# Performance work log

Hardware: AMD Instinct MI355X
Metric: run time of the kernel (lower is better)

## Reference

```python
import jax, jax.numpy as jnp
import numpy as np

E = 128   # embedding_dim
H = 4     # num_heads
D = E * H # internal width = 512 (MHA head_dim = E)
B = 512
N = 128


def setup_inputs() -> dict:
    key = jax.random.key(0)
    ks = jax.random.split(key, 16)
    s = lambda fan_in: 1.0 / np.sqrt(fan_in)
    u = lambda k, shape, sc: jax.random.uniform(k, shape, jnp.float32, -sc, sc)
    inp = {
        "x": jax.random.normal(ks[0], (B, N, E), jnp.float32),
        "weights": jax.random.uniform(ks[1], (B, N, 1), jnp.float32),
        # self.embedding: Linear(E, D)
        "emb_W": u(ks[2], (D, E), s(E)), "emb_b": u(ks[3], (D,), s(E)),
        # outer W_q/W_k/W_v: Linear(D, D)
        "wq_W": u(ks[4], (D, D), s(D)), "wq_b": u(ks[5], (D,), s(D)),
        "wk_W": u(ks[6], (D, D), s(D)), "wk_b": u(ks[7], (D,), s(D)),
        "wv_W": u(ks[8], (D, D), s(D)), "wv_b": u(ks[9], (D,), s(D)),
        # nn.MultiheadAttention packed in-projection (out_proj is irrelevant:
        # its output is discarded, only att_weights are used)
        "in_proj_W": u(ks[10], (3 * D, D), s(D)),
        "in_proj_b": jnp.zeros((3 * D,), jnp.float32),
        # LayerNorm(D)
        "ln_g": jnp.ones((D,), jnp.float32), "ln_b": jnp.zeros((D,), jnp.float32),
        # self.out: Linear(D, E)
        "out_W": u(ks[11], (E, D), s(D)), "out_b": u(ks[12], (E,), s(D)),
    }
    return inp


def reference(x, weights, emb_W, emb_b, wq_W, wq_b, wk_W, wk_b, wv_W, wv_b,
              in_proj_W, in_proj_b, ln_g, ln_b, out_W, out_b):
    # x: [B, N, E] -> embedded [B, N, D]
    xe = x @ emb_W.T + emb_b
    # key_padding_mask: rows of xe that are all-zero
    pad = jnp.sum(jnp.abs(xe), axis=-1) == 0.0              # [B, N] bool

    # outer projections
    q_in = xe @ wq_W.T + wq_b
    k_in = xe @ wk_W.T + wk_b
    v_in = xe @ wv_W.T + wv_b                               # [B, N, D]

    # MHA internal packed in-projection
    Wq, Wk, Wv = in_proj_W[:D], in_proj_W[D:2 * D], in_proj_W[2 * D:]
    bq, bk, bv = in_proj_b[:D], in_proj_b[D:2 * D], in_proj_b[2 * D:]
    hd = D // H  # head_dim = E
    to_heads = lambda t: t.reshape(t.shape[0], t.shape[1], H, hd).transpose(0, 2, 1, 3)
    q = to_heads(q_in @ Wq.T + bq)                          # [B, H, N, hd]
    k = to_heads(k_in @ Wk.T + bk)

    scores = jnp.einsum('bhie,bhje->bhij', q, k) / jnp.sqrt(jnp.float32(hd))
    scores = jnp.where(pad[:, None, None, :], -jnp.inf, scores)
    attn = jax.nn.softmax(scores, axis=-1)                  # [B, H, N, N]
    att_weights = jnp.mean(attn, axis=1)                    # averaged over heads [B, N, N]

    # external reweighting + renormalization
    att_weights = att_weights * jnp.swapaxes(weights, -2, -1)  # [B,N,N]*[B,1,N]
    att_weights = att_weights / jnp.sum(att_weights, axis=-1, keepdims=True)

    # re-apply to outer V projection (MHA's own output is discarded)
    att_output = jnp.einsum('bij,bjd->bid', att_weights, v_in)

    h = xe + jax.nn.softplus(att_output)
    mu = jnp.mean(h, axis=-1, keepdims=True)
    var = jnp.mean((h - mu) ** 2, axis=-1, keepdims=True)
    h = (h - mu) / jnp.sqrt(var + 1e-5) * ln_g + ln_b
    return h @ out_W.T + out_b                              # [B, N, E]
```

## Files before the change

kernel.cpp:

```cpp
#include <hip/hip_runtime.h>
#include <stdint.h>


typedef __attribute__((ext_vector_type(8))) __bf16 bf16x8;
typedef __attribute__((ext_vector_type(8))) uint16_t u16x8;
typedef __attribute__((ext_vector_type(4))) float f32x4;

__device__ __forceinline__ float b2f(uint16_t h) {
  union { uint32_t u; float f; } c; c.u = ((uint32_t)h) << 16; return c.f;
}
__device__ __forceinline__ uint16_t f2b(float f) {
  __bf16 h = (__bf16)f;
  union { __bf16 b; uint16_t u; } c; c.b = h; return c.u;
}
__device__ __forceinline__ void gld16(void* lds, const void* g) {
  __builtin_amdgcn_global_load_lds(
      (const __attribute__((address_space(1))) uint32_t*)(g),
      (__attribute__((address_space(3))) uint32_t*)(lds),
      16, 0, 0);
}

#define MFMA16(a, b, c) __builtin_amdgcn_mfma_f32_16x16x32_bf16((a), (b), (c), 0, 0, 0)

__global__ __launch_bounds__(256) void pack_all(
    const float* __restrict__ x,
    const float* __restrict__ emb_W, const float* __restrict__ wq_W,
    const float* __restrict__ wk_W, const float* __restrict__ wv_W,
    const float* __restrict__ ipW, const float* __restrict__ out_W,
    const float* __restrict__ ln_g,
    uint16_t* __restrict__ x_bf,
    uint16_t* __restrict__ embW2, uint16_t* __restrict__ wqW_bf,
    uint16_t* __restrict__ wkW_bf, uint16_t* __restrict__ Wvc,
    uint16_t* __restrict__ ip_bf, uint16_t* __restrict__ owW_bf) {
  int i = blockIdx.x * 256 + threadIdx.x;
  if (i < 2097152) {
    float4 v = ((const float4*)x)[i];
    ushort4 o;
    o.x = f2b(v.x); o.y = f2b(v.y); o.z = f2b(v.z); o.w = f2b(v.w);
    ((ushort4*)x_bf)[i] = o;
    return;
  }
  int i2 = i - 2097152;
  if (i2 >= 360448) return;
  if (i2 >= 344064) {
    const int off = i2 - 344064;
    float4 v = ((const float4*)out_W)[off];
    const int base = off * 4;
    ushort4 o;
    o.x = f2b(v.x * ln_g[(base + 0) & 511]);
    o.y = f2b(v.y * ln_g[(base + 1) & 511]);
    o.z = f2b(v.z * ln_g[(base + 2) & 511]);
    o.w = f2b(v.w * ln_g[(base + 3) & 511]);
    ((ushort4*)owW_bf)[off] = o;
    return;
  }
  const float* src; uint16_t* dst; int off;
  if (i2 < 16384)       { src = emb_W; dst = embW2;  off = i2; }
  else if (i2 < 81920)  { src = wq_W;  dst = wqW_bf; off = i2 - 16384; }
  else if (i2 < 147456) { src = wk_W;  dst = wkW_bf; off = i2 - 81920; }
  else if (i2 < 212992) { src = wv_W;  dst = Wvc;    off = i2 - 147456; }
  else                  { src = ipW;   dst = ip_bf;  off = i2 - 212992; }
  float4 v = ((const float4*)src)[off];
  ushort4 o;
  o.x = f2b(v.x); o.y = f2b(v.y); o.z = f2b(v.z); o.w = f2b(v.w);
  ((ushort4*)dst)[off] = o;
}

__global__ __launch_bounds__(256) void bias_stage1(
    const float* __restrict__ wq_W, const float* __restrict__ wk_W,
    const float* __restrict__ wv_W, const float* __restrict__ emb_b,
    const float* __restrict__ wq_b, const float* __restrict__ wk_b,
    const float* __restrict__ wv_b,
    float* __restrict__ t1q, float* __restrict__ t1k, float* __restrict__ bve,
    float* __restrict__ pad_init, float* __restrict__ biasE,
    float* __restrict__ ssum, float* __restrict__ ssq) {
  const int gid = blockIdx.x * 256 + threadIdx.x;
  if (gid < 65536) { pad_init[gid] = 0.f; ssum[gid] = 0.f; ssq[gid] = 0.f; }
  if (gid < 512) biasE[gid] = emb_b[gid];
  const int t = threadIdx.x, l = t & 63, w = t >> 6;
  const int sel = blockIdx.x >> 7;
  const int row = (blockIdx.x & 127) * 4 + w;
  const float* Wbig = sel == 0 ? wq_W : (sel == 1 ? wk_W : wv_W);
  const float* b2   = sel == 0 ? wq_b : (sel == 1 ? wk_b : wv_b);
  float* out        = sel == 0 ? t1q  : (sel == 1 ? t1k  : bve);
  float s = 0.f;
  #pragma unroll
  for (int j = 0; j < 8; ++j) {
    int c = j * 64 + l;
    s += Wbig[(size_t)row * 512 + c] * emb_b[c];
  }
  #pragma unroll
  for (int m = 1; m < 64; m <<= 1) s += __shfl_xor(s, m);
  if (l == 0) out[row] = s + b2[row];
}

__global__ __launch_bounds__(256) void bias_stage2(
    const float* __restrict__ ipW, const float* __restrict__ ipb,
    const float* __restrict__ t1q, const float* __restrict__ t1k,
    float* __restrict__ bqe, float* __restrict__ bke,
    const float* __restrict__ out_W, const float* __restrict__ ln_g,
    const float* __restrict__ ln_b, const float* __restrict__ out_b,
    float* __restrict__ u, float* __restrict__ v) {
  const int t = threadIdx.x, l = t & 63, w = t >> 6;
  const int blk = blockIdx.x;
  if (blk < 256) {
    const int sel = blk >> 7;
    const int row = (blk & 127) * 4 + w;
    const float* Wbig = ipW + (size_t)sel * 262144;
    const float* b1   = sel == 0 ? t1q : t1k;
    const float* b2   = ipb + sel * 512;
    float* out        = sel == 0 ? bqe : bke;
    float s = 0.f;
    #pragma unroll
    for (int j = 0; j < 8; ++j) {
      int c = j * 64 + l;
      s += Wbig[(size_t)row * 512 + c] * b1[c];
    }
    #pragma unroll
    for (int m = 1; m < 64; m <<= 1) s += __shfl_xor(s, m);
    if (l == 0) out[row] = s + b2[row];
  } else {
    const int r4 = (blk - 256) * 4 + w;
    const int row = r4 & 127;
    const float* src = (r4 < 128) ? ln_g : ln_b;
    float s = 0.f;
    #pragma unroll
    for (int j = 0; j < 8; ++j) {
      int c = j * 64 + l;
      s += out_W[(size_t)row * 512 + c] * src[c];
    }
    #pragma unroll
    for (int m = 1; m < 64; m <<= 1) s += __shfl_xor(s, m);
    if (l == 0) {
      if (r4 < 128) u[row] = s;
      else v[row] = s + out_b[row];
    }
  }
}

template <int BIAS_MODE, bool PAD_ACC, bool HV>
__global__ __launch_bounds__(256) void gemm_btp_kernel(
    const uint16_t* __restrict__ A, long long sA,
    const uint16_t* __restrict__ W, long long sW,
    const float* __restrict__ bias, long long sBias,
    uint16_t* __restrict__ C, long long sC,
    int mIter, float* __restrict__ padout,
    const uint16_t* __restrict__ xein, float* __restrict__ ssum,
    float* __restrict__ ssq) {
  __shared__ uint16_t Ws[2][128 * 64];
  __shared__ uint16_t As[2][128 * 64];
  const int t = threadIdx.x, l = t & 63, w = t >> 6;
  const int wr = w >> 1, wc = w & 1, l15 = l & 15, hi = l >> 4;
  const int gx = gridDim.x, gy = gridDim.y;
  const int nwg = gx * gy * gridDim.z;
  const int lin = blockIdx.x + gx * (blockIdx.y + gy * blockIdx.z);
  const int cpx = nwg >> 3;
  const int sw = (nwg & 7) ? lin : ((lin & 7) * cpx + (lin >> 3));
  const int ntile = sw % gx;
  const int rest = sw / gx;
  const int mg = rest % gy, bz = rest / gy;
  const uint16_t* Ab = A + (size_t)bz * sA;
  const uint16_t* Wb = W + (size_t)bz * sW;
  uint16_t* Cb = C + (size_t)bz * sC;
  const float* biasb = bias + (size_t)bz * sBias;
  const int srow = t >> 3;
  const int schunk = (t & 7) * 8;
  const int gchunk = (((t & 7) ^ (srow & 7)) * 8);
  const int rowB0 = ntile * 128;
  #pragma unroll
  for (int kt = 0; kt < 2; ++kt)
    #pragma unroll
    for (int i = 0; i < 4; ++i) {
      const int r = i * 32 + srow;
      gld16(&Ws[kt][r * 64 + schunk], Wb + (size_t)(rowB0 + r) * 128 + kt * 64 + gchunk);
    }
  auto stageA = [&](int u) {
    const int rowA0 = (mg * mIter + (u >> 1)) * 128;
    const int kb = (u & 1) << 6;
    #pragma unroll
    for (int i = 0; i < 4; ++i) {
      const int r = i * 32 + srow;
      gld16(&As[u & 1][r * 64 + schunk], Ab + (size_t)(rowA0 + r) * 128 + kb + gchunk);
    }
  };
  const int rsw = (l15 & 7);
  stageA(0);
  const int U = mIter * 2;
  f32x4 acc[4][4];
  for (int u = 0; u < U; ++u) {
    const int kt = u & 1;
    if (kt == 0) {
      #pragma unroll
      for (int m = 0; m < 4; ++m)
        #pragma unroll
        for (int n = 0; n < 4; ++n) acc[m][n] = (f32x4){0.f, 0.f, 0.f, 0.f};
    }
    if (u + 1 < U) {
      stageA(u + 1);
      asm volatile("s_waitcnt vmcnt(4)" ::: "memory");
    } else {
      asm volatile("s_waitcnt vmcnt(0)" ::: "memory");
    }
    __builtin_amdgcn_s_barrier();
    asm volatile("" ::: "memory");
    #pragma unroll
    for (int ks = 0; ks < 2; ++ks) {
      const int gck = ((ks * 4 + hi) ^ rsw) * 8;
      bf16x8 a[4], bb[4];
      #pragma unroll
      for (int m = 0; m < 4; ++m)
        a[m] = *(const bf16x8*)&As[kt][(wr * 64 + m * 16 + l15) * 64 + gck];
      #pragma unroll
      for (int n = 0; n < 4; ++n)
        bb[n] = *(const bf16x8*)&Ws[kt][(wc * 64 + n * 16 + l15) * 64 + gck];
      #pragma unroll
      for (int m = 0; m < 4; ++m)
        #pragma unroll
        for (int n = 0; n < 4; ++n) acc[m][n] = MFMA16(bb[n], a[m], acc[m][n]);
    }
    asm volatile("" ::: "memory");
    __builtin_amdgcn_s_barrier();
    if (kt == 1) {
      const int rowA0 = (mg * mIter + (u >> 1)) * 128;
      #pragma unroll
      for (int m = 0; m < 4; ++m) {
        const int row = rowA0 + wr * 64 + m * 16 + l15;
        float padp = 0.f, hs = 0.f, hq = 0.f;
        #pragma unroll
        for (int n = 0; n < 4; ++n) {
          const int colb = rowB0 + wc * 64 + n * 16 + hi * 4;
          union { ushort4 v; uint16_t e[4]; } o, xv;
          if constexpr (HV)
            xv.v = *(const ushort4*)&xein[(size_t)row * 512 + colb];
          #pragma unroll
          for (int r = 0; r < 4; ++r) {
            float rv = acc[m][n][r];
            if constexpr (BIAS_MODE == 1) rv += biasb[colb + r];
            if constexpr (PAD_ACC) padp += fabsf(rv);
            if constexpr (HV) {
              const float sp = fmaxf(rv, 0.f) + __logf(1.f + __expf(-fabsf(rv)));
              const float hvv = b2f(xv.e[r]) + sp;
              hs += hvv;
              hq += hvv * hvv;
              o.e[r] = f2b(hvv);
            } else {
              o.e[r] = f2b(rv);
            }
          }
          *(ushort4*)&Cb[(size_t)row * 512 + colb] = o.v;
        }
        if constexpr (PAD_ACC) {
          if (bz == 0) {
            padp += __shfl_xor(padp, 16);
            padp += __shfl_xor(padp, 32);
            if (l < 16) atomicAdd(padout + row, padp);
          }
        }
        if constexpr (HV) {
          hs += __shfl_xor(hs, 16); hs += __shfl_xor(hs, 32);
          hq += __shfl_xor(hq, 16); hq += __shfl_xor(hq, 32);
          if (l < 16) {
            atomicAdd(ssum + row, hs);
            atomicAdd(ssq + row, hq);
          }
        }
      }
    }
  }
}

template <typename OT, int BIAS_MODE, bool LN>
__global__ __launch_bounds__(256) void gemm_bt_kernel(
    const uint16_t* __restrict__ A, long long sA,
    const uint16_t* __restrict__ W, long long sW,
    const float* __restrict__ bias, long long sBias,
    OT* __restrict__ C, long long sC, int N, int K,
    const float* __restrict__ ssum, const float* __restrict__ ssq,
    const float* __restrict__ uarr, const float* __restrict__ varr) {
  __shared__ uint16_t As[2][128 * 64];
  __shared__ uint16_t Bs[2][128 * 64];
  const int t = threadIdx.x, l = t & 63, w = t >> 6;
  const int wr = w >> 1, wc = w & 1, l15 = l & 15, hi = l >> 4;
  const int gx = gridDim.x, gy = gridDim.y;
  const int nwg = gx * gy * gridDim.z;
  const int lin = blockIdx.x + gx * (blockIdx.y + gy * blockIdx.z);
  const int cpx = nwg >> 3;
  const int sw = (nwg & 7) ? lin : ((lin & 7) * cpx + (lin >> 3));
  const int ntile = sw % gx;
  const int rest = sw / gx;
  const int mtile = rest % gy, bz = rest / gy;
  const uint16_t* Ab = A + (size_t)bz * sA;
  const uint16_t* Wb = W + (size_t)bz * sW;
  OT* Cb = C + (size_t)bz * sC;
  const float* biasb = bias + (size_t)bz * sBias;
  f32x4 acc[4][4];
  #pragma unroll
  for (int m = 0; m < 4; ++m)
    #pragma unroll
    for (int n = 0; n < 4; ++n) acc[m][n] = (f32x4){0.f, 0.f, 0.f, 0.f};
  const int srow = t >> 3;
  const int schunk = (t & 7) * 8;
  const int gchunk = (((t & 7) ^ (srow & 7)) * 8);
  const int nk = K >> 6;
  const int rowA0 = mtile * 128, rowB0 = ntile * 128;
  auto stage = [&](int kt, int buf) {
    const int kb = kt << 6;
    #pragma unroll
    for (int i = 0; i < 4; ++i) {
      const int r = i * 32 + srow;
      gld16(&As[buf][r * 64 + schunk], Ab + (size_t)(rowA0 + r) * K + kb + gchunk);
      gld16(&Bs[buf][r * 64 + schunk], Wb + (size_t)(rowB0 + r) * K + kb + gchunk);
    }
  };
  stage(0, 0);
  const int rsw = (l15 & 7);
  for (int kt = 0; kt < nk; ++kt) {
    const int cur = kt & 1;
    if (kt + 1 < nk) {
      stage(kt + 1, cur ^ 1);
      asm volatile("s_waitcnt vmcnt(8)" ::: "memory");
    } else {
      asm volatile("s_waitcnt vmcnt(0)" ::: "memory");
    }
    __builtin_amdgcn_s_barrier();
    asm volatile("" ::: "memory");
    #pragma unroll
    for (int ks = 0; ks < 2; ++ks) {
      const int gck = ((ks * 4 + hi) ^ rsw) * 8;
      bf16x8 a[4], bb[4];
      #pragma unroll
      for (int m = 0; m < 4; ++m)
        a[m] = *(const bf16x8*)&As[cur][(wr * 64 + m * 16 + l15) * 64 + gck];
      #pragma unroll
      for (int n = 0; n < 4; ++n)
        bb[n] = *(const bf16x8*)&Bs[cur][(wc * 64 + n * 16 + l15) * 64 + gck];
      #pragma unroll
      for (int m = 0; m < 4; ++m)
        #pragma unroll
        for (int n = 0; n < 4; ++n) acc[m][n] = MFMA16(bb[n], a[m], acc[m][n]);
    }
    asm volatile("" ::: "memory");
    __builtin_amdgcn_s_barrier();
  }
  #pragma unroll
  for (int m = 0; m < 4; ++m) {
    const int row = rowA0 + wr * 64 + m * 16 + l15;
    float mu = 0.f, rstd = 0.f;
    if constexpr (LN) {
      mu = ssum[row] * (1.f / 512.f);
      const float var = ssq[row] * (1.f / 512.f) - mu * mu;
      rstd = rsqrtf(var + 1e-5f);
    }
    #pragma unroll
    for (int n = 0; n < 4; ++n) {
      const int colb = rowB0 + wc * 64 + n * 16 + hi * 4;
      if constexpr (sizeof(OT) == 2) {
        union { ushort4 v; uint16_t e[4]; } o;
        #pragma unroll
        for (int r = 0; r < 4; ++r) {
          float rv;
          if constexpr (LN) {
            rv = rstd * (acc[m][n][r] - mu * uarr[colb + r]) + varr[colb + r];
          } else {
            float bv = 0.f;
            if constexpr (BIAS_MODE == 1) bv = biasb[colb + r];
            rv = acc[m][n][r] + bv;
          }
          o.e[r] = f2b(rv);
        }
        *(ushort4*)&((uint16_t*)Cb)[(size_t)row * N + colb] = o.v;
      } else {
        union { float4 v; float e[4]; } o;
        #pragma unroll
        for (int r = 0; r < 4; ++r) {
          float rv;
          if constexpr (LN) {
            rv = rstd * (acc[m][n][r] - mu * uarr[colb + r]) + varr[colb + r];
          } else {
            float bv = 0.f;
            if constexpr (BIAS_MODE == 1) bv = biasb[colb + r];
            rv = acc[m][n][r] + bv;
          }
          o.e[r] = rv;
        }
        *(float4*)&Cb[(size_t)row * N + colb] = o.v;
      }
    }
  }
}

__global__ __launch_bounds__(256) void gemm_ab_kernel(
    const uint16_t* __restrict__ A, int lda, long long sA,
    const uint16_t* __restrict__ B, int ldb, long long sB,
    uint16_t* __restrict__ C, int ldc, long long sC, int K) {
  __shared__ uint16_t As[128 * 64];
  __shared__ uint16_t Bt[128 * 64];
  const int t = threadIdx.x, l = t & 63, w = t >> 6;
  const int wr = w >> 1, wc = w & 1, l15 = l & 15, hi = l >> 4;
  const int gx = gridDim.x, gy = gridDim.y;
  const int nwg = gx * gy * gridDim.z;
  const int lin = blockIdx.x + gx * (blockIdx.y + gy * blockIdx.z);
  const int cpx = nwg >> 3;
  const int sw = (nwg & 7) ? lin : ((lin & 7) * cpx + (lin >> 3));
  const int ntile = sw % gx;
  const int rest = sw / gx;
  const int mtile = rest % gy, bz = rest / gy;
  const uint16_t* Ab = A + (size_t)bz * sA;
  const uint16_t* Bb = B + (size_t)bz * sB;
  uint16_t* Cb = C + (size_t)bz * sC;
  f32x4 acc[4][4];
  #pragma unroll
  for (int m = 0; m < 4; ++m)
    #pragma unroll
    for (int n = 0; n < 4; ++n) acc[m][n] = (f32x4){0.f, 0.f, 0.f, 0.f};
  const int srow = t >> 3, schunk = (t & 7) * 8;
  const int nk = K >> 6;
  for (int kt = 0; kt < nk; ++kt) {
    const int kb = kt << 6;
    #pragma unroll
    for (int i = 0; i < 4; ++i) {
      const int r = i * 32 + srow;
      gld16(&As[r * 64 + schunk], Ab + (size_t)(mtile * 128 + r) * lda + kb + schunk);
    }
    #pragma unroll
    for (int rd = 0; rd < 4; ++rd) {
      const int id = rd * 256 + t;
      const int kr = id >> 4;
      const int c = (id & 15) * 8;
      u16x8 gv = *(const u16x8*)(Bb + (size_t)(kb + kr) * ldb + ntile * 128 + c);
      #pragma unroll
      for (int j = 0; j < 8; ++j) Bt[(c + j) * 64 + kr] = gv[j];
    }
    __syncthreads();
    #pragma unroll
    for (int ks = 0; ks < 2; ++ks) {
      const int k0 = ks * 32 + hi * 8;
      bf16x8 a[4], bb[4];
      #pragma unroll
      for (int m = 0; m < 4; ++m) a[m] = *(const bf16x8*)&As[(wr * 64 + m * 16 + l15) * 64 + k0];
      #pragma unroll
      for (int n = 0; n < 4; ++n) bb[n] = *(const bf16x8*)&Bt[(wc * 64 + n * 16 + l15) * 64 + k0];
      #pragma unroll
      for (int m = 0; m < 4; ++m)
        #pragma unroll
        for (int n = 0; n < 4; ++n) acc[m][n] = MFMA16(a[m], bb[n], acc[m][n]);
    }
    __syncthreads();
  }
  #pragma unroll
  for (int m = 0; m < 4; ++m) {
    const int row = mtile * 128 + wr * 64 + m * 16 + hi * 4;
    #pragma unroll
    for (int n = 0; n < 4; ++n) {
      const int col = ntile * 128 + wc * 64 + n * 16 + l15;
      #pragma unroll
      for (int r = 0; r < 4; ++r)
        Cb[(size_t)(row + r) * ldc + col] = f2b(acc[m][n][r]);
    }
  }
}

__global__ __launch_bounds__(256) void gemm_atb_kernel(
    const uint16_t* __restrict__ Wke, const uint16_t* __restrict__ Wqe,
    const float* __restrict__ bqe, uint16_t* __restrict__ Wg,
    float* __restrict__ vh) {
  __shared__ uint16_t At[128 * 64];
  __shared__ uint16_t Bt[128 * 64];
  const int h = blockIdx.x;
  const int t = threadIdx.x, l = t & 63, w = t >> 6;
  const int wr = w >> 1, wc = w & 1, l15 = l & 15, hi = l >> 4;
  const uint16_t* A = Wke + (size_t)h * 16384;
  const uint16_t* B = Wqe + (size_t)h * 16384;
  f32x4 acc[4][4];
  #pragma unroll
  for (int m = 0; m < 4; ++m)
    #pragma unroll
    for (int n = 0; n < 4; ++n) acc[m][n] = (f32x4){0.f, 0.f, 0.f, 0.f};
  float vacc = 0.f;
  for (int kt = 0; kt < 2; ++kt) {
    const int kb = kt << 6;
    #pragma unroll
    for (int rd = 0; rd < 4; ++rd) {
      const int id = rd * 256 + t;
      const int kr = id >> 4;
      const int c = (id & 15) * 8;
      u16x8 ga = *(const u16x8*)(A + (size_t)(kb + kr) * 128 + c);
      u16x8 gb = *(const u16x8*)(B + (size_t)(kb + kr) * 128 + c);
      #pragma unroll
      for (int j = 0; j < 8; ++j) {
        const int row = c + j;
        const int sxz = (((row & 7) ^ ((row >> 3) & 7)) << 3);
        At[row * 64 + (kr ^ sxz)] = ga[j];
        Bt[row * 64 + (kr ^ sxz)] = gb[j];
      }
    }
    __syncthreads();
    if (t < 128) {
      const int sxz = (((t & 7) ^ ((t >> 3) & 7)) << 3);
      for (int o = 0; o < 64; ++o)
        vacc += b2f(At[t * 64 + (o ^ sxz)]) * bqe[h * 128 + kb + o];
    }
    #pragma unroll
    for (int ks = 0; ks < 2; ++ks) {
      bf16x8 a[4], bb[4];
      #pragma unroll
      for (int m = 0; m < 4; ++m) {
        const int mr = wr * 64 + m * 16 + l15;
        const int sxz = (((mr & 7) ^ ((mr >> 3) & 7)) << 3);
        a[m] = *(const bf16x8*)&At[mr * 64 + ((ks * 32 + hi * 8) ^ sxz)];
      }
      #pragma unroll
      for (int n = 0; n < 4; ++n) {
        const int nr = wc * 64 + n * 16 + l15;
        const int sxz = (((nr & 7) ^ ((nr >> 3) & 7)) << 3);
        bb[n] = *(const bf16x8*)&Bt[nr * 64 + ((ks * 32 + hi * 8) ^ sxz)];
      }
      #pragma unroll
      for (int m = 0; m < 4; ++m)
        #pragma unroll
        for (int n = 0; n < 4; ++n) acc[m][n] = MFMA16(a[m], bb[n], acc[m][n]);
    }
    __syncthreads();
  }
  if (t < 128) vh[h * 128 + t] = vacc;
  #pragma unroll
  for (int m = 0; m < 4; ++m) {
    const int row = wr * 64 + m * 16 + hi * 4;
    #pragma unroll
    for (int n = 0; n < 4; ++n) {
      const int col = wc * 64 + n * 16 + l15;
      #pragma unroll
      for (int r = 0; r < 4; ++r)
        Wg[(size_t)h * 16384 + (size_t)(row + r) * 128 + col] = f2b(acc[m][n][r]);
    }
  }
}

__global__ __launch_bounds__(512) void att_fused(
    const uint16_t* __restrict__ xg, const uint16_t* __restrict__ Wg,
    const float* __restrict__ vh, const float* __restrict__ wts,
    const float* __restrict__ padsum, uint16_t* __restrict__ tout) {
  __shared__ uint16_t Xr[2][128 * 64];
  __shared__ uint16_t GP[2][128 * 64];
  __shared__ float bS[4][128];
  const int blk = blockIdx.x;
  const int b = (blk & 7) * 64 + (blk >> 3);
  const int t = threadIdx.x, l = t & 63, wband = t >> 6;
  const int l15 = l & 15, hi = l >> 4;
  const int srow = t >> 3;
  const int schunk = (t & 7) * 8;
  const int gchunk = (((t & 7) ^ (srow & 7)) * 8);
  const float SCALE = 0.088388347648318447f;
  const int rsw = (l15 & 7);

  const uint16_t* xb = xg + (size_t)b * 16384;
  #pragma unroll
  for (int kt = 0; kt < 2; ++kt)
    #pragma unroll
    for (int i = 0; i < 2; ++i) {
      const int r = i * 64 + srow;
      gld16(&Xr[kt][r * 64 + schunk], xb + (size_t)r * 128 + kt * 64 + gchunk);
      gld16(&GP[kt][r * 64 + schunk], Wg + (size_t)r * 128 + kt * 64 + gchunk);
    }
  asm volatile("s_waitcnt vmcnt(0)" ::: "memory");
  __builtin_amdgcn_s_barrier();
  {
    const int hh = t >> 7, j = t & 127;
    float s = 0.f;
    for (int e = 0; e < 128; ++e) {
      const int c = e & 63;
      const int addr = j * 64 + ((((c >> 3) ^ (j & 7)) << 3) | (c & 7));
      s += b2f(Xr[e >> 6][addr]) * vh[hh * 128 + e];
    }
    bS[hh][j] = s * SCALE +
                ((padsum[(size_t)b * 128 + j] == 0.f) ? -__builtin_inff() : 0.f);
  }

  f32x4 awacc[8];
  #pragma unroll
  for (int n = 0; n < 8; ++n) awacc[n] = (f32x4){0.f, 0.f, 0.f, 0.f};
  u16x8 wreg[4];
  u16x8 xtr[4];

  for (int h = 0; h < 4; ++h) {
    f32x4 pacc[8];
    #pragma unroll
    for (int n = 0; n < 8; ++n) pacc[n] = (f32x4){0.f, 0.f, 0.f, 0.f};
    __builtin_amdgcn_s_setprio(1);
    #pragma unroll
    for (int kt = 0; kt < 2; ++kt)
      #pragma unroll
      for (int ks = 0; ks < 2; ++ks) {
        const int gck = ((ks * 4 + hi) ^ rsw) * 8;
        bf16x8 a, bb[8];
        a = *(const bf16x8*)&Xr[kt][(wband * 16 + l15) * 64 + gck];
        #pragma unroll
        for (int n = 0; n < 8; ++n)
          bb[n] = *(const bf16x8*)&GP[kt][(n * 16 + l15) * 64 + gck];
        #pragma unroll
        for (int n = 0; n < 8; ++n) pacc[n] = MFMA16(a, bb[n], pacc[n]);
      }
    __builtin_amdgcn_s_setprio(0);
    if (h + 1 < 4) {
      #pragma unroll
      for (int kt = 0; kt < 2; ++kt)
        #pragma unroll
        for (int i = 0; i < 2; ++i) {
          const int r = i * 64 + srow;
          wreg[kt * 2 + i] = *(const u16x8*)(Wg + (size_t)(h + 1) * 16384 +
                                             (size_t)r * 128 + kt * 64 + gchunk);
        }
    }
    __builtin_amdgcn_s_barrier();
    #pragma unroll
    for (int n = 0; n < 8; ++n) {
      const int cl = n * 16 + l15;
      const int c = cl & 63;
      #pragma unroll
      for (int r = 0; r < 4; ++r) {
        const int rr = wband * 16 + hi * 4 + r;
        GP[cl >> 6][rr * 64 + ((((c >> 3) ^ (rr & 7)) << 3) | (c & 7))] =
            f2b(pacc[n][r]);
      }
    }
    __builtin_amdgcn_s_barrier();
    f32x4 sacc[8];
    #pragma unroll
    for (int n = 0; n < 8; ++n) sacc[n] = (f32x4){0.f, 0.f, 0.f, 0.f};
    __builtin_amdgcn_s_setprio(1);
    #pragma unroll
    for (int kt = 0; kt < 2; ++kt)
      #pragma unroll
      for (int ks = 0; ks < 2; ++ks) {
        const int gck = ((ks * 4 + hi) ^ rsw) * 8;
        bf16x8 a, bb[8];
        a = *(const bf16x8*)&GP[kt][(wband * 16 + l15) * 64 + gck];
        #pragma unroll
        for (int n = 0; n < 8; ++n)
          bb[n] = *(const bf16x8*)&Xr[kt][(n * 16 + l15) * 64 + gck];
        #pragma unroll
        for (int n = 0; n < 8; ++n) sacc[n] = MFMA16(a, bb[n], sacc[n]);
      }
    __builtin_amdgcn_s_setprio(0);
    if (h == 3) {
      #pragma unroll
      for (int i = 0; i < 4; ++i) {
        const int id = i * 512 + t;
        const int jr = id >> 4;
        const int cc = (id & 15) * 8;
        xtr[i] = *(const u16x8*)(xb + (size_t)jr * 128 + cc);
      }
    }
    #pragma unroll
    for (int r = 0; r < 4; ++r) {
      float e[8], z = 0.f;
      #pragma unroll
      for (int n = 0; n < 8; ++n) {
        e[n] = __expf(sacc[n][r] * SCALE + bS[h][n * 16 + l15]);
        z += e[n];
      }
      z += __shfl_xor(z, 1); z += __shfl_xor(z, 2);
      z += __shfl_xor(z, 4); z += __shfl_xor(z, 8);
      const float zi = 1.f / z;
      #pragma unroll
      for (int n = 0; n < 8; ++n) awacc[n][r] += e[n] * zi;
    }
    if (h + 1 < 4) {
      __builtin_amdgcn_s_barrier();
      asm volatile("s_waitcnt vmcnt(0)" ::: "memory");
      #pragma unroll
      for (int kt = 0; kt < 2; ++kt)
        #pragma unroll
        for (int i = 0; i < 2; ++i) {
          const int r = i * 64 + srow;
          *(u16x8*)&GP[kt][r * 64 + schunk] = wreg[kt * 2 + i];
        }
      __builtin_amdgcn_s_barrier();
    }
  }
  float wv[8];
  #pragma unroll
  for (int n = 0; n < 8; ++n) wv[n] = wts[(size_t)b * 128 + n * 16 + l15];
  __builtin_amdgcn_s_barrier();
  #pragma unroll
  for (int r = 0; r < 4; ++r) {
    float z = 0.f;
    #pragma unroll
    for (int n = 0; n < 8; ++n) z += awacc[n][r] * wv[n];
    z += __shfl_xor(z, 1); z += __shfl_xor(z, 2);
    z += __shfl_xor(z, 4); z += __shfl_xor(z, 8);
    const float zi = 1.f / z;
    const int rr = wband * 16 + hi * 4 + r;
    #pragma unroll
    for (int n = 0; n < 8; ++n) {
      const int cl = n * 16 + l15;
      const int c = cl & 63;
      GP[cl >> 6][rr * 64 + ((((c >> 3) ^ (rr & 7)) << 3) | (c & 7))] =
          f2b(awacc[n][r] * wv[n] * zi);
    }
  }
  asm volatile("s_waitcnt vmcnt(0)" ::: "memory");
  #pragma unroll
  for (int i = 0; i < 4; ++i) {
    const int id = i * 512 + t;
    const int jr = id >> 4;
    const int cc = (id & 15) * 8;
    const int kt2 = jr >> 6, kr = jr & 63;
    #pragma unroll
    for (int j = 0; j < 8; ++j) {
      const int drow = cc + j;
      const int sxz = (((drow & 7) ^ ((drow >> 3) & 7)) << 3);
      Xr[kt2][drow * 64 + (kr ^ sxz)] = xtr[i][j];
    }
  }
  __builtin_amdgcn_s_barrier();
  f32x4 tacc[8];
  #pragma unroll
  for (int n = 0; n < 8; ++n) tacc[n] = (f32x4){0.f, 0.f, 0.f, 0.f};
  __builtin_amdgcn_s_setprio(1);
  #pragma unroll
  for (int kt = 0; kt < 2; ++kt)
    #pragma unroll
    for (int ks = 0; ks < 2; ++ks) {
      const int gck = ((ks * 4 + hi) ^ rsw) * 8;
      bf16x8 a, bb[8];
      a = *(const bf16x8*)&GP[kt][(wband * 16 + l15) * 64 + gck];
      #pragma unroll
      for (int n = 0; n < 8; ++n) {
        const int nr = n * 16 + l15;
        const int sxz = (((nr & 7) ^ ((nr >> 3) & 7)) << 3);
        bb[n] = *(const bf16x8*)&Xr[kt][nr * 64 + ((ks * 32 + hi * 8) ^ sxz)];
      }
      #pragma unroll
      for (int n = 0; n < 8; ++n) tacc[n] = MFMA16(a, bb[n], tacc[n]);
    }
  __builtin_amdgcn_s_setprio(0);
  #pragma unroll
  for (int r = 0; r < 4; ++r) {
    const int row = wband * 16 + hi * 4 + r;
    #pragma unroll
    for (int n = 0; n < 8; ++n) {
      const int col = n * 16 + l15;
      tout[(size_t)b * 16384 + (size_t)row * 128 + col] = f2b(tacc[n][r]);
    }
  }
}

extern "C" void kernel_launch(void* const* d_in, const int* in_sizes, int n_in,
                              void* d_out, int out_size, void* d_ws, size_t ws_size,
                              hipStream_t stream) {
  (void)in_sizes; (void)n_in; (void)out_size; (void)ws_size;
  const float* x     = (const float*)d_in[0];
  const float* wts   = (const float*)d_in[1];
  const float* emb_W = (const float*)d_in[2];
  const float* emb_b = (const float*)d_in[3];
  const float* wq_W  = (const float*)d_in[4];
  const float* wq_b  = (const float*)d_in[5];
  const float* wk_W  = (const float*)d_in[6];
  const float* wk_b  = (const float*)d_in[7];
  const float* wv_W  = (const float*)d_in[8];
  const float* wv_b  = (const float*)d_in[9];
  const float* ipW   = (const float*)d_in[10];
  const float* ipb   = (const float*)d_in[11];
  const float* ln_g  = (const float*)d_in[12];
  const float* ln_b  = (const float*)d_in[13];
  const float* out_W = (const float*)d_in[14];
  const float* out_b = (const float*)d_in[15];

  char* ws = (char*)d_ws;
  size_t off = 0;
  auto alloc = [&](size_t bytes) { void* p = ws + off; off += (bytes + 255) & ~(size_t)255; return p; };
  uint16_t* wqW_bf = (uint16_t*)alloc(524288);
  uint16_t* wkW_bf = (uint16_t*)alloc(524288);
  uint16_t* ip_bf  = (uint16_t*)alloc(1048576);
  uint16_t* owW_bf = (uint16_t*)alloc(131072);
  uint16_t* Wqc    = (uint16_t*)alloc(524288);
  uint16_t* Wkc    = (uint16_t*)alloc(524288);
  uint16_t* Wvc    = (uint16_t*)alloc(524288);
  uint16_t* embW2  = (uint16_t*)alloc(131072);
  uint16_t* Wqe    = (uint16_t*)alloc(131072);
  uint16_t* Wke    = (uint16_t*)alloc(131072);
  uint16_t* Wve    = (uint16_t*)alloc(131072);
  uint16_t* Wg     = (uint16_t*)alloc(131072);
  float*    vhbuf  = (float*)alloc(2048);
  float*    t1q    = (float*)alloc(2048);
  float*    t1k    = (float*)alloc(2048);
  float*    biasE  = (float*)alloc(2048);
  float*    bqe    = (float*)alloc(2048);
  float*    bke    = (float*)alloc(2048);
  float*    bve    = (float*)alloc(2048);
  float*    uarr   = (float*)alloc(2048);
  float*    varr   = (float*)alloc(2048);
  float*    pad    = (float*)alloc(262144);
  float*    ssum   = (float*)alloc(262144);
  float*    ssq    = (float*)alloc(262144);
  uint16_t* xe     = (uint16_t*)alloc(67108864);
  uint16_t* B1     = (uint16_t*)alloc(67108864);
  uint16_t* B2     = (uint16_t*)alloc(67108864);

  uint16_t* x_bf = (uint16_t*)d_out + 8388608;
  uint16_t* tb   = B1;
  uint16_t* hv   = B2;

  const int TB = 256;
  pack_all<<<9600, TB, 0, stream>>>(x, emb_W, wq_W, wk_W, wv_W, ipW, out_W, ln_g,
                                    x_bf, embW2, wqW_bf, wkW_bf, Wvc, ip_bf, owW_bf);
  bias_stage1<<<384, TB, 0, stream>>>(wq_W, wk_W, wv_W, emb_b, wq_b, wk_b, wv_b,
                                      t1q, t1k, bve, pad, biasE, ssum, ssq);
  bias_stage2<<<320, TB, 0, stream>>>(ipW, ipb, t1q, t1k, bqe, bke,
                                      out_W, ln_g, ln_b, out_b, uarr, varr);
  gemm_ab_kernel<<<dim3(4, 4, 2), TB, 0, stream>>>(ip_bf, 512, 262144, wqW_bf, 512, 262144,
                                                   Wqc, 512, 262144, 512);
  gemm_ab_kernel<<<dim3(1, 4, 3), TB, 0, stream>>>(Wqc, 512, 262144, embW2, 128, 0,
                                                   Wqe, 128, 65536, 512);
  gemm_atb_kernel<<<4, TB, 0, stream>>>(Wke, Wqe, bqe, Wg, vhbuf);
  gemm_btp_kernel<1, true, false><<<dim3(4, 128, 1), TB, 0, stream>>>(
      x_bf, 0, embW2, 0, biasE, 0, xe, 0, 4, pad, nullptr, nullptr, nullptr);
  att_fused<<<512, 512, 0, stream>>>(x_bf, Wg, vhbuf, wts, pad, tb);
  gemm_btp_kernel<1, false, true><<<dim3(4, 128, 1), TB, 0, stream>>>(
      tb, 0, Wve, 0, bve, 0, hv, 0, 4, nullptr, xe, ssum, ssq);
  gemm_bt_kernel<float, 0, true><<<dim3(1, 512, 1), TB, 0, stream>>>(
      hv, 0, owW_bf, 0, nullptr, 0, (float*)d_out, 0, 128, 512,
      ssum, ssq, uarr, varr);
}
```

Baseline: 221.3 us.

## Load A fragments directly from global memory in persistent-weight GEMM

The A-tile LDS staging and double-buffered pipeline in gemm_btp_kernel are removed. Each wave now reads its A fragments straight from global memory into registers, and only the W tile stays in shared memory. This halves LDS use so the kernel can declare three blocks per CU, and it drops the per-step barriers. In exchange, global loads are uncoalesced 16-byte row-strided reads with no prefetch overlap, so the MFMAs may stall on memory latency.

```diff
diff --git a/kernel.cpp b/kernel.cpp
--- a/kernel.cpp
+++ b/kernel.cpp
@@ -139,7 +139,7 @@
 }
 
 template <int BIAS_MODE, bool PAD_ACC, bool HV>
-__global__ __launch_bounds__(256) void gemm_btp_kernel(
+__global__ __launch_bounds__(256, 3) void gemm_btp_kernel(
     const uint16_t* __restrict__ A, long long sA,
     const uint16_t* __restrict__ W, long long sW,
     const float* __restrict__ bias, long long sBias,
@@ -148,7 +148,6 @@
     const uint16_t* __restrict__ xein, float* __restrict__ ssum,
     float* __restrict__ ssq) {
   __shared__ uint16_t Ws[2][128 * 64];
-  __shared__ uint16_t As[2][128 * 64];
   const int t = threadIdx.x, l = t & 63, w = t >> 6;
   const int wr = w >> 1, wc = w & 1, l15 = l & 15, hi = l >> 4;
   const int gx = gridDim.x, gy = gridDim.y;
@@ -174,95 +173,74 @@
       const int r = i * 32 + srow;
       gld16(&Ws[kt][r * 64 + schunk], Wb + (size_t)(rowB0 + r) * 128 + kt * 64 + gchunk);
     }
-  auto stageA = [&](int u) {
-    const int rowA0 = (mg * mIter + (u >> 1)) * 128;
-    const int kb = (u & 1) << 6;
-    #pragma unroll
-    for (int i = 0; i < 4; ++i) {
-      const int r = i * 32 + srow;
-      gld16(&As[u & 1][r * 64 + schunk], Ab + (size_t)(rowA0 + r) * 128 + kb + gchunk);
-    }
-  };
+  asm volatile("s_waitcnt vmcnt(0)" ::: "memory");
+  __syncthreads();
   const int rsw = (l15 & 7);
-  stageA(0);
-  const int U = mIter * 2;
-  f32x4 acc[4][4];
-  for (int u = 0; u < U; ++u) {
-    const int kt = u & 1;
-    if (kt == 0) {
-      #pragma unroll
-      for (int m = 0; m < 4; ++m)
-        #pragma unroll
-        for (int n = 0; n < 4; ++n) acc[m][n] = (f32x4){0.f, 0.f, 0.f, 0.f};
-    }
-    if (u + 1 < U) {
-      stageA(u + 1);
-      asm volatile("s_waitcnt vmcnt(4)" ::: "memory");
-    } else {
-      asm volatile("s_waitcnt vmcnt(0)" ::: "memory");
-    }
-    __builtin_amdgcn_s_barrier();
-    asm volatile("" ::: "memory");
-    #pragma unroll
-    for (int ks = 0; ks < 2; ++ks) {
-      const int gck = ((ks * 4 + hi) ^ rsw) * 8;
-      bf16x8 a[4], bb[4];
-      #pragma unroll
-      for (int m = 0; m < 4; ++m)
-        a[m] = *(const bf16x8*)&As[kt][(wr * 64 + m * 16 + l15) * 64 + gck];
-      #pragma unroll
-      for (int n = 0; n < 4; ++n)
-        bb[n] = *(const bf16x8*)&Ws[kt][(wc * 64 + n * 16 + l15) * 64 + gck];
-      #pragma unroll
-      for (int m = 0; m < 4; ++m)
-        #pragma unroll
-        for (int n = 0; n < 4; ++n) acc[m][n] = MFMA16(bb[n], a[m], acc[m][n]);
-    }
-    asm volatile("" ::: "memory");
-    __builtin_amdgcn_s_barrier();
-    if (kt == 1) {
-      const int rowA0 = (mg * mIter + (u >> 1)) * 128;
-      #pragma unroll
-      for (int m = 0; m < 4; ++m) {
-        const int row = rowA0 + wr * 64 + m * 16 + l15;
-        float padp = 0.f, hs = 0.f, hq = 0.f;
-        #pragma unroll
-        for (int n = 0; n < 4; ++n) {
-          const int colb = rowB0 + wc * 64 + n * 16 + hi * 4;
-          union { ushort4 v; uint16_t e[4]; } o, xv;
-          if constexpr (HV)
-            xv.v = *(const ushort4*)&xein[(size_t)row * 512 + colb];
+  for (int it = 0; it < mIter; ++it) {
+    const int rowA0 = (mg * mIter + it) * 128;
+    f32x4 acc[4][4];
+    #pragma unroll
+    for (int m = 0; m < 4; ++m)
+      #pragma unroll
+      for (int n = 0; n < 4; ++n) acc[m][n] = (f32x4){0.f, 0.f, 0.f, 0.f};
+    #pragma unroll
+    for (int kt = 0; kt < 2; ++kt)
+      #pragma unroll
+      for (int ks = 0; ks < 2; ++ks) {
+        const int gck = ((ks * 4 + hi) ^ rsw) * 8;
+        bf16x8 bb[4];
+        #pragma unroll
+        for (int n = 0; n < 4; ++n)
+          bb[n] = *(const bf16x8*)&Ws[kt][(wc * 64 + n * 16 + l15) * 64 + gck];
+        #pragma unroll
+        for (int m = 0; m < 4; ++m) {
+          bf16x8 a = *(const bf16x8*)(Ab +
+              (size_t)(rowA0 + wr * 64 + m * 16 + l15) * 128 +
+              kt * 64 + (ks * 4 + hi) * 8);
           #pragma unroll
-          for (int r = 0; r < 4; ++r) {
-            float rv = acc[m][n][r];
-            if constexpr (BIAS_MODE == 1) rv += biasb[colb + r];
-            if constexpr (PAD_ACC) padp += fabsf(rv);
-            if constexpr (HV) {
-              const float sp = fmaxf(rv, 0.f) + __logf(1.f + __expf(-fabsf(rv)));
-              const float hvv = b2f(xv.e[r]) + sp;
-              hs += hvv;
-              hq += hvv * hvv;
-              o.e[r] = f2b(hvv);
-            } else {
-              o.e[r] = f2b(rv);
-            }
-          }
-          *(ushort4*)&Cb[(size_t)row * 512 + colb] = o.v;
+          for (int n = 0; n < 4; ++n) acc[m][n] = MFMA16(bb[n], a, acc[m][n]);
         }
-        if constexpr (PAD_ACC) {
-          if (bz == 0) {
-            padp += __shfl_xor(padp, 16);
-            padp += __shfl_xor(padp, 32);
-            if (l < 16) atomicAdd(padout + row, padp);
+      }
+    #pragma unroll
+    for (int m = 0; m < 4; ++m) {
+      const int row = rowA0 + wr * 64 + m * 16 + l15;
+      float padp = 0.f, hs = 0.f, hq = 0.f;
+      #pragma unroll
+      for (int n = 0; n < 4; ++n) {
+        const int colb = rowB0 + wc * 64 + n * 16 + hi * 4;
+        union { ushort4 v; uint16_t e[4]; } o, xv;
+        if constexpr (HV)
+          xv.v = *(const ushort4*)&xein[(size_t)row * 512 + colb];
+        #pragma unroll
+        for (int r = 0; r < 4; ++r) {
+          float rv = acc[m][n][r];
+          if constexpr (BIAS_MODE == 1) rv += biasb[colb + r];
+          if constexpr (PAD_ACC) padp += fabsf(rv);
+          if constexpr (HV) {
+            const float sp = fmaxf(rv, 0.f) + __logf(1.f + __expf(-fabsf(rv)));
+            const float hvv = b2f(xv.e[r]) + sp;
+            hs += hvv;
+            hq += hvv * hvv;
+            o.e[r] = f2b(hvv);
+          } else {
+            o.e[r] = f2b(rv);
           }
         }
-        if constexpr (HV) {
-          hs += __shfl_xor(hs, 16); hs += __shfl_xor(hs, 32);
-          hq += __shfl_xor(hq, 16); hq += __shfl_xor(hq, 32);
-          if (l < 16) {
-            atomicAdd(ssum + row, hs);
-            atomicAdd(ssq + row, hq);
-          }
+        *(ushort4*)&Cb[(size_t)row * 512 + colb] = o.v;
+      }
+      if constexpr (PAD_ACC) {
+        if (bz == 0) {
+          padp += __shfl_xor(padp, 16);
+          padp += __shfl_xor(padp, 32);
+          if (l < 16) atomicAdd(padout + row, padp);
+        }
+      }
+      if constexpr (HV) {
+        hs += __shfl_xor(hs, 16); hs += __shfl_xor(hs, 32);
+        hq += __shfl_xor(hq, 16); hq += __shfl_xor(hq, 32);
+        if (l < 16) {
+          atomicAdd(ssum + row, hs);
+          atomicAdd(ssq + row, hq);
         }
       }
     }
```

Measured after the change: 275.6 us. +24.6%, slower.
